# Performance work log

Measured on AMD Instinct MI355X. Metric: run time of the kernel, lower is better.

The kernel has to match this reference:

```python
import jax, jax.numpy as jnp
import numpy as np

N, E, F, H, EA = 50000, 500000, 2000, 128, 2
NUM_BOND_TYPES = 100
COORDS_RANGE = 10.0
NORM_FACTOR = 100.0


def setup_inputs() -> dict:
    key = jax.random.key(0)
    ks = jax.random.split(key, 20)

    def lin(k, i, o, gain=1.0):
        # xavier-uniform-ish init, stored as [in, out] so forward is x @ W + b
        lim = gain * np.sqrt(6.0 / (i + o))
        return jax.random.uniform(k, (i, o), jnp.float32, -lim, lim)

    inp = {
        "h_a": jax.random.normal(ks[0], (N, H), jnp.float32),
        "x_a": jax.random.normal(ks[1], (N, 3), jnp.float32),
        "e_a_idx": jax.random.randint(ks[2], (2, E), 0, N),
        "e_a_type": jax.random.randint(ks[3], (E,), 0, NUM_BOND_TYPES),
        "e_a_attr": jax.random.normal(ks[4], (E, EA), jnp.float32),
        "coord_diff_a": jax.random.normal(ks[5], (E, 3), jnp.float32),
        "h_f": jax.random.normal(ks[6], (F, H), jnp.float32),
        "x_f": jax.random.normal(ks[7], (F, 3), jnp.float32),
        "bm_mat": jax.random.normal(ks[8], (N, F), jnp.float32) / np.sqrt(F),
        # parameters
        "bond_emb": jax.random.normal(ks[9], (NUM_BOND_TYPES, H), jnp.float32),
        "aW1": lin(ks[10], 2 * H + EA + H, H), "ab1": jnp.zeros((H,), jnp.float32),
        "aW2": lin(ks[11], H, H), "ab2": jnp.zeros((H,), jnp.float32),
        "aW3": lin(ks[12], H, 1, gain=0.001),  # xavier gain=0.001, no bias
        "fW1": lin(ks[13], 2 * H + EA, H), "fb1": jnp.zeros((H,), jnp.float32),
        "fW2": lin(ks[14], H, H), "fb2": jnp.zeros((H,), jnp.float32),
        "fW3": lin(ks[15], H, 1, gain=0.001),
    }
    return inp


def reference(h_a, x_a, e_a_idx, e_a_type, e_a_attr, coord_diff_a, h_f, x_f, bm_mat,
              bond_emb, aW1, ab1, aW2, ab2, aW3, fW1, fb1, fW2, fb2, fW3):
    silu = jax.nn.silu
    row, col = e_a_idx[0], e_a_idx[1]

    be = bond_emb[e_a_type]                              # [E, H]
    coord_diff_f = x_a - bm_mat @ x_f                    # [N, 3]
    radial_f = jnp.sum(coord_diff_f ** 2, axis=1, keepdims=True)  # [N, 1]
    norm_f = jnp.sqrt(radial_f + 1e-8)
    coord_diff_f = coord_diff_f / (norm_f + 1.0)

    inp_atom = jnp.concatenate([h_a[row], h_a[col], e_a_attr, be], axis=1)        # [E, 3H+2]
    inp_frag = jnp.concatenate([h_a, bm_mat @ h_f, radial_f, radial_f], axis=1)   # [N, 2H+2]

    m_atom = silu(silu(inp_atom @ aW1 + ab1) @ aW2 + ab2) @ aW3  # [E, 1]
    m_frag = silu(silu(inp_frag @ fW1 + fb1) @ fW2 + fb2) @ fW3  # [N, 1]

    trans_atom = coord_diff_a * jnp.tanh(m_atom) * COORDS_RANGE  # [E, 3]
    trans_frag = coord_diff_f * jnp.tanh(m_frag) * COORDS_RANGE  # [N, 3]

    agg_atom = jax.ops.segment_sum(trans_atom, row, num_segments=x_a.shape[0]) / NORM_FACTOR
    return x_a + agg_atom + trans_frag
```

## Files before the change

### kernel.cpp

```cpp
#include <hip/hip_runtime.h>
#include <hip/hip_bf16.h>


typedef __attribute__((ext_vector_type(8))) short bfrag8;
typedef __attribute__((ext_vector_type(16))) float f32x16;
typedef __attribute__((ext_vector_type(4))) float f32x4v;

#define MFMA32(A, B, C) __builtin_amdgcn_mfma_f32_32x32x16_bf16((A), (B), (C), 0, 0, 0)

__device__ __forceinline__ f32x16 zero16() {
  f32x16 v;
#pragma unroll
  for (int i = 0; i < 16; ++i) v[i] = 0.0f;
  return v;
}

__device__ __forceinline__ unsigned short bf16bits(float x) {
  __hip_bfloat16 b = __float2bfloat16(x);
  unsigned short u;
  __builtin_memcpy(&u, &b, 2);
  return u;
}

__device__ __forceinline__ unsigned pk2(float lo, float hi) {
  return (unsigned)bf16bits(lo) | ((unsigned)bf16bits(hi) << 16);
}

__device__ __forceinline__ bfrag8 ldfrag(const unsigned short* p) {
  return *reinterpret_cast<const bfrag8*>(p);
}

__device__ __forceinline__ bfrag8 frag4(unsigned f0, unsigned f1, unsigned f2, unsigned f3) {
  union { unsigned u[4]; bfrag8 v; } q;
  q.u[0] = f0; q.u[1] = f1; q.u[2] = f2; q.u[3] = f3;
  return q.v;
}

__device__ __forceinline__ float silu_f(float x) { return x / (1.0f + __expf(-x)); }

__global__ __launch_bounds__(256) void prep_kernel(
    const float* __restrict__ h_a, const float* __restrict__ bond,
    const float* __restrict__ h_f,
    const float* __restrict__ aW1, const float* __restrict__ ab1,
    const float* __restrict__ aW2,
    const float* __restrict__ fW1, const float* __restrict__ fW2,
    unsigned short* __restrict__ h_bf, unsigned short* __restrict__ bond_bf,
    float* __restrict__ hfp,
    unsigned short* __restrict__ W1aT, unsigned short* __restrict__ W1bT,
    unsigned short* __restrict__ W1cT, unsigned short* __restrict__ W1eT,
    unsigned short* __restrict__ W2T,
    unsigned short* __restrict__ fW1aT, unsigned short* __restrict__ fW2T,
    float* __restrict__ agg,
    int N, int NB, int F) {
  const int t = threadIdx.x;
  int bid = blockIdx.x;
  const int G_A = (N * 16 + 255) >> 8;
  const int G_B = (NB * 16 + 255) >> 8;
  const int G_H = (F + 1) >> 1;

  if (bid < G_A + G_B) {
    const float* src = (bid < G_A) ? h_a : bond;
    unsigned short* dst = (bid < G_A) ? h_bf : bond_bf;
    int rows = (bid < G_A) ? N : NB;
    int idx = (bid < G_A ? bid : bid - G_A) * 256 + t;
    if (idx < rows * 16) {
      int row = idx >> 4, g = idx & 15;
      int h = g & 1, kc = g >> 1;
      const f32x4v* s = reinterpret_cast<const f32x4v*>(src + (size_t)row * 128 + g * 8);
      f32x4v v0 = s[0], v1 = s[1];
      unsigned* d = reinterpret_cast<unsigned*>(dst + (size_t)row * 128 + h * 64 + kc * 8);
      d[0] = pk2(v0[0], v0[1]);
      d[1] = pk2(v0[2], v0[3]);
      d[2] = pk2(v1[0], v1[1]);
      d[3] = pk2(v1[2], v1[3]);
    }
    return;
  }
  bid -= G_A + G_B;
  if (bid < G_H) {
    int f = bid * 2 + (t >> 7), n = t & 127;
    if (f < F) {
      float acc = 0.0f;
#pragma unroll 8
      for (int k = 0; k < 128; ++k)
        acc += h_f[(size_t)f * 128 + k] * fW1[(size_t)(128 + k) * 128 + n];
      hfp[(size_t)f * 128 + n] = acc;
    }
    return;
  }
  bid -= G_H;
  if (bid < 6 * 64) {
    int p = bid >> 6;
    int tt = (bid & 63) * 256 + t;
    int j = tt & 7, l = (tt >> 3) & 63, rem = tt >> 9;
    int nt = rem & 3, kc = rem >> 2;
    int k = kc * 16 + ((l >> 5) << 3) + j;
    int n = nt * 32 + (l & 31);
    const float* W;
    unsigned short* D;
    switch (p) {
      case 0: W = aW1;             D = W1aT;  break;
      case 1: W = aW1 + 128 * 128; D = W1bT;  break;
      case 2: W = aW1 + 258 * 128; D = W1cT;  break;
      case 3: W = aW2;             D = W2T;   break;
      case 4: W = fW1;             D = fW1aT; break;
      default: W = fW2;            D = fW2T;  break;
    }
    D[tt] = bf16bits(W[(size_t)k * 128 + n]);
    return;
  }
  bid -= 6 * 64;
  if (bid < 8) {
    int tt = bid * 256 + t;
    if (tt < 4 * 64 * 8) {
      int j = tt & 7, l = (tt >> 3) & 63, nt = (tt >> 9) & 3;
      int k = ((l >> 5) << 3) + j;
      int n = nt * 32 + (l & 31);
      float v = (k == 0) ? aW1[(size_t)256 * 128 + n]
              : (k == 1) ? aW1[(size_t)257 * 128 + n]
              : (k == 2) ? ab1[n] : 0.0f;
      W1eT[tt] = bf16bits(v);
    }
    return;
  }
  bid -= 8;
  {
    int i4 = (bid * 256 + t) * 4;
    if (i4 + 3 < N * 3) {
      *reinterpret_cast<f32x4v*>(agg + i4) = f32x4v{0.f, 0.f, 0.f, 0.f};
    } else {
      for (int c = 0; c < 4; ++c)
        if (i4 + c < N * 3) agg[i4 + c] = 0.0f;
    }
  }
}

__global__ void pack_bmat_kernel(const float* __restrict__ hfp, const float* __restrict__ x_f,
                                 unsigned short* __restrict__ dst, int total) {
  int t = blockIdx.x * blockDim.x + threadIdx.x;
  if (t >= total) return;
  int j = t & 7, l = (t >> 3) & 63, rem = t >> 9;
  int nt = rem % 5, kc = rem / 5;
  int k = kc * 16 + ((l >> 5) << 3) + j;
  int n = nt * 32 + (l & 31);
  float v;
  if (n < 128) v = hfp[(size_t)k * 128 + n];
  else if (n < 131) v = x_f[(size_t)k * 3 + (n - 128)];
  else v = 0.0f;
  dst[t] = bf16bits(v);
}

__global__ __launch_bounds__(256, 2) void fused_k1_k3(
    const float* __restrict__ bm, const unsigned short* __restrict__ bmT,
    float* __restrict__ k1T,
    const unsigned short* __restrict__ h_bf, const unsigned short* __restrict__ bond_bf,
    const int* __restrict__ eidx, const int* __restrict__ etype,
    const float* __restrict__ eattr, const float* __restrict__ cda,
    const unsigned short* __restrict__ W1aT, const unsigned short* __restrict__ W1bT,
    const unsigned short* __restrict__ W1cT, const unsigned short* __restrict__ W1eT,
    const unsigned short* __restrict__ W2T,
    const float* __restrict__ ab2, const float* __restrict__ aW3,
    float* __restrict__ agg,
    int N, int F, int E, int G1) {
  __shared__ __align__(16) char lds[2][128 * 128];
  const int lane = threadIdx.x & 63;
  const int w = threadIdx.x >> 6;
  const int h = lane >> 5;
  const int ln = lane & 31;

  if ((int)blockIdx.x < G1) {
    const int t = threadIdx.x;
    const int m0 = blockIdx.x * 128;
    const int NT = (F + 63) >> 6;

    f32x16 acc[5];
#pragma unroll
    for (int i = 0; i < 5; ++i) acc[i] = zero16();

    int srow[8], sch[8];
    const float* sptr[8];
#pragma unroll
    for (int p = 0; p < 8; ++p) {
      int c = p * 256 + t;
      srow[p] = c >> 4;
      sch[p] = c & 15;
      int gr = m0 + srow[p];
      if (gr >= N) gr = N - 1;
      sptr[p] = bm + (size_t)gr * F;
    }

    const int myrow = w * 32 + ln;
    const int rsw = (myrow & 7) << 4;

    f32x4v sregs[8];
#pragma unroll
    for (int p = 0; p < 8; ++p) {
      int gk = sch[p] * 4;
      if (gk > F - 4) gk = F - 4;
      sregs[p] = *reinterpret_cast<const f32x4v*>(sptr[p] + gk);
    }
#pragma unroll
    for (int p = 0; p < 8; ++p) {
      int byte = srow[p] * 128 + ((sch[p] * 8) ^ ((srow[p] & 7) << 4));
      union { unsigned u[2]; unsigned long long ull; } q;
      q.u[0] = pk2(sregs[p][0], sregs[p][1]);
      q.u[1] = pk2(sregs[p][2], sregs[p][3]);
      *reinterpret_cast<unsigned long long*>(&lds[0][byte]) = q.ull;
    }
    __syncthreads();

    int cur = 0;
    for (int kt = 0; kt < NT; ++kt) {
      const bool more = (kt + 1 < NT);
      if (more) {
#pragma unroll
        for (int p = 0; p < 8; ++p) {
          int gk = (kt + 1) * 64 + sch[p] * 4;
          if (gk > F - 4) gk = F - 4;
          sregs[p] = *reinterpret_cast<const f32x4v*>(sptr[p] + gk);
        }
      }
      const int rem = (F - kt * 64) >> 4;
      const int kcN = rem < 4 ? rem : 4;
      if (kcN == 4) {
#pragma unroll
        for (int kc = 0; kc < 4; ++kc) {
          bfrag8 b = *reinterpret_cast<const bfrag8*>(
              &lds[cur][myrow * 128 + ((kc * 32 + h * 16) ^ rsw)]);
          const unsigned short* wp = bmT + ((size_t)(kt * 4 + kc) * 5 * 64 + lane) * 8;
#pragma unroll
          for (int nt = 0; nt < 5; ++nt) acc[nt] = MFMA32(ldfrag(wp + nt * 512), b, acc[nt]);
        }
      } else {
        for (int kc = 0; kc < kcN; ++kc) {
          bfrag8 b = *reinterpret_cast<const bfrag8*>(
              &lds[cur][myrow * 128 + ((kc * 32 + h * 16) ^ rsw)]);
          const unsigned short* wp = bmT + ((size_t)(kt * 4 + kc) * 5 * 64 + lane) * 8;
#pragma unroll
          for (int nt = 0; nt < 5; ++nt) acc[nt] = MFMA32(ldfrag(wp + nt * 512), b, acc[nt]);
        }
      }
      if (more) {
#pragma unroll
        for (int p = 0; p < 8; ++p) {
          int byte = srow[p] * 128 + ((sch[p] * 8) ^ ((srow[p] & 7) << 4));
          union { unsigned u[2]; unsigned long long ull; } q;
          q.u[0] = pk2(sregs[p][0], sregs[p][1]);
          q.u[1] = pk2(sregs[p][2], sregs[p][3]);
          *reinterpret_cast<unsigned long long*>(&lds[cur ^ 1][byte]) = q.ull;
        }
      }
      __syncthreads();
      cur ^= 1;
    }

    const int m = m0 + myrow;
    if (m < N) {
#pragma unroll
      for (int nt = 0; nt < 5; ++nt)
#pragma unroll
        for (int r = 0; r < 16; ++r) {
          int n = nt * 32 + (r & 3) + 8 * (r >> 2) + 4 * h;
          if (n < 131) k1T[(size_t)n * N + m] = acc[nt][r];
        }
    }
    return;
  }

  const int e = (blockIdx.x - G1) * 128 + w * 32 + ln;
  const bool valid = (e < E);
  const int ec = valid ? e : (E - 1);
  const int row = eidx[ec];
  const int col = eidx[(size_t)E + ec];
  const int typ = etype[ec];
  const float e0 = eattr[2 * (size_t)ec];
  const float e1 = eattr[2 * (size_t)ec + 1];

  const unsigned short* hr = h_bf + (size_t)row * 128 + h * 64;
  const unsigned short* hc = h_bf + (size_t)col * 128 + h * 64;
  const unsigned short* bb = bond_bf + (size_t)typ * 128 + h * 64;

  f32x16 acc[4];
#pragma unroll
  for (int q = 0; q < 4; ++q) acc[q] = zero16();

#pragma unroll
  for (int kc = 0; kc < 8; ++kc) {
    bfrag8 b = ldfrag(hr + kc * 8);
    const unsigned short* wp = W1aT + ((size_t)(kc * 4) * 64 + lane) * 8;
#pragma unroll
    for (int nt = 0; nt < 4; ++nt) acc[nt] = MFMA32(ldfrag(wp + nt * 512), b, acc[nt]);
  }
#pragma unroll
  for (int kc = 0; kc < 8; ++kc) {
    bfrag8 b = ldfrag(hc + kc * 8);
    const unsigned short* wp = W1bT + ((size_t)(kc * 4) * 64 + lane) * 8;
#pragma unroll
    for (int nt = 0; nt < 4; ++nt) acc[nt] = MFMA32(ldfrag(wp + nt * 512), b, acc[nt]);
  }
#pragma unroll
  for (int kc = 0; kc < 8; ++kc) {
    bfrag8 b = ldfrag(bb + kc * 8);
    const unsigned short* wp = W1cT + ((size_t)(kc * 4) * 64 + lane) * 8;
#pragma unroll
    for (int nt = 0; nt < 4; ++nt) acc[nt] = MFMA32(ldfrag(wp + nt * 512), b, acc[nt]);
  }
  {
    unsigned u0 = h ? 0u : pk2(e0, e1);
    unsigned u1 = h ? 0u : 0x00003F80u;
    bfrag8 b = frag4(u0, u1, 0u, 0u);
    const unsigned short* wp = W1eT + (size_t)lane * 8;
#pragma unroll
    for (int nt = 0; nt < 4; ++nt) acc[nt] = MFMA32(ldfrag(wp + nt * 512), b, acc[nt]);
  }

  unsigned wv[32];
#pragma unroll
  for (int nt = 0; nt < 4; ++nt)
#pragma unroll
    for (int p = 0; p < 8; ++p)
      wv[nt * 8 + p] = pk2(silu_f(acc[nt][2 * p]), silu_f(acc[nt][2 * p + 1]));

#pragma unroll
  for (int q = 0; q < 4; ++q) acc[q] = zero16();
#pragma unroll
  for (int kc = 0; kc < 8; ++kc) {
    const int base = (kc >> 1) * 8 + (kc & 1) * 4;
    unsigned a0 = wv[base + 0], a1 = wv[base + 1], a2 = wv[base + 2], a3 = wv[base + 3];
    unsigned s0 = (unsigned)__shfl_xor((int)a0, 32);
    unsigned s1 = (unsigned)__shfl_xor((int)a1, 32);
    unsigned s2 = (unsigned)__shfl_xor((int)a2, 32);
    unsigned s3 = (unsigned)__shfl_xor((int)a3, 32);
    bfrag8 b = frag4(h ? s2 : a0, h ? s3 : a1, h ? a2 : s0, h ? a3 : s1);
    const unsigned short* wp = W2T + ((size_t)(kc * 4) * 64 + lane) * 8;
#pragma unroll
    for (int nt = 0; nt < 4; ++nt) acc[nt] = MFMA32(ldfrag(wp + nt * 512), b, acc[nt]);
  }

  float part = 0.0f;
#pragma unroll
  for (int nt = 0; nt < 4; ++nt)
#pragma unroll
    for (int r = 0; r < 16; ++r) {
      int n = nt * 32 + (r & 3) + 8 * (r >> 2) + 4 * h;
      part += silu_f(acc[nt][r] + ab2[n]) * aW3[n];
    }
  float mv = part + __shfl_xor(part, 32);

  if (valid) {
    float tt = tanhf(mv) * 0.1f;
    if (h == 0) {
      atomicAdd(agg + 3 * (size_t)row + 0, cda[3 * (size_t)ec + 0] * tt);
      atomicAdd(agg + 3 * (size_t)row + 1, cda[3 * (size_t)ec + 1] * tt);
    } else {
      atomicAdd(agg + 3 * (size_t)row + 2, cda[3 * (size_t)ec + 2] * tt);
    }
  }
}

__global__ __launch_bounds__(256) void k2_frag(
    const float* __restrict__ x_a, const unsigned short* __restrict__ h_bf,
    const float* __restrict__ k1T, const float* __restrict__ agg,
    const unsigned short* __restrict__ fW1aT, const unsigned short* __restrict__ fW2T,
    const float* __restrict__ fW1, const float* __restrict__ fb1,
    const float* __restrict__ fb2, const float* __restrict__ fW3,
    float* __restrict__ out, int N) {
  const int lane = threadIdx.x & 63;
  const int wid = threadIdx.x >> 6;
  const int h = lane >> 5;
  const int ln = lane & 31;
  const int i = blockIdx.x * 128 + wid * 32 + ln;
  const bool valid = (i < N);
  const int ic = valid ? i : (N - 1);

  float cd[3];
  float radial = 0.0f;
#pragma unroll
  for (int c = 0; c < 3; ++c) {
    float v = x_a[3 * (size_t)ic + c] - k1T[(size_t)(128 + c) * N + ic];
    cd[c] = v;
    radial += v * v;
  }

  f32x16 acc[4];
#pragma unroll
  for (int q = 0; q < 4; ++q) acc[q] = zero16();
  const unsigned short* hp = h_bf + (size_t)ic * 128 + h * 64;
#pragma unroll
  for (int kc = 0; kc < 8; ++kc) {
    bfrag8 b = ldfrag(hp + kc * 8);
    const unsigned short* wp = fW1aT + ((size_t)(kc * 4) * 64 + lane) * 8;
#pragma unroll
    for (int nt = 0; nt < 4; ++nt) acc[nt] = MFMA32(ldfrag(wp + nt * 512), b, acc[nt]);
  }

  unsigned wv[32];
#pragma unroll
  for (int nt = 0; nt < 4; ++nt)
#pragma unroll
    for (int p = 0; p < 8; ++p) {
      const int r0 = 2 * p;
      const int n0 = nt * 32 + (r0 & 3) + 8 * (r0 >> 2) + 4 * h;
      const int n1 = n0 + 1;
      float q0 = acc[nt][r0] + k1T[(size_t)n0 * N + ic]
               + radial * (fW1[(size_t)256 * 128 + n0] + fW1[(size_t)257 * 128 + n0]) + fb1[n0];
      float q1 = acc[nt][r0 + 1] + k1T[(size_t)n1 * N + ic]
               + radial * (fW1[(size_t)256 * 128 + n1] + fW1[(size_t)257 * 128 + n1]) + fb1[n1];
      wv[nt * 8 + p] = pk2(silu_f(q0), silu_f(q1));
    }

#pragma unroll
  for (int q = 0; q < 4; ++q) acc[q] = zero16();
#pragma unroll
  for (int kc = 0; kc < 8; ++kc) {
    const int base = (kc >> 1) * 8 + (kc & 1) * 4;
    unsigned a0 = wv[base + 0], a1 = wv[base + 1], a2 = wv[base + 2], a3 = wv[base + 3];
    unsigned s0 = (unsigned)__shfl_xor((int)a0, 32);
    unsigned s1 = (unsigned)__shfl_xor((int)a1, 32);
    unsigned s2 = (unsigned)__shfl_xor((int)a2, 32);
    unsigned s3 = (unsigned)__shfl_xor((int)a3, 32);
    bfrag8 b = frag4(h ? s2 : a0, h ? s3 : a1, h ? a2 : s0, h ? a3 : s1);
    const unsigned short* wp = fW2T + ((size_t)(kc * 4) * 64 + lane) * 8;
#pragma unroll
    for (int nt = 0; nt < 4; ++nt) acc[nt] = MFMA32(ldfrag(wp + nt * 512), b, acc[nt]);
  }

  float part = 0.0f;
#pragma unroll
  for (int nt = 0; nt < 4; ++nt)
#pragma unroll
    for (int r = 0; r < 16; ++r) {
      int n = nt * 32 + (r & 3) + 8 * (r >> 2) + 4 * h;
      part += silu_f(acc[nt][r] + fb2[n]) * fW3[n];
    }
  float mv = part + __shfl_xor(part, 32);

  if (valid && h == 0) {
    float nrm = sqrtf(radial + 1e-8f);
    float s = tanhf(mv) * 10.0f / (nrm + 1.0f);
#pragma unroll
    for (int c = 0; c < 3; ++c)
      out[3 * (size_t)i + c] = x_a[3 * (size_t)i + c] + cd[c] * s + agg[3 * (size_t)i + c];
  }
}


extern "C" void kernel_launch(void* const* d_in, const int* in_sizes, int n_in,
                              void* d_out, int out_size, void* d_ws, size_t ws_size,
                              hipStream_t stream) {
  const float* h_a    = (const float*)d_in[0];
  const float* x_a    = (const float*)d_in[1];
  const int*   e_idx  = (const int*)d_in[2];
  const int*   e_type = (const int*)d_in[3];
  const float* e_attr = (const float*)d_in[4];
  const float* cda    = (const float*)d_in[5];
  const float* h_f    = (const float*)d_in[6];
  const float* x_f    = (const float*)d_in[7];
  const float* bm     = (const float*)d_in[8];
  const float* bond   = (const float*)d_in[9];
  const float* aW1    = (const float*)d_in[10];
  const float* ab1    = (const float*)d_in[11];
  const float* aW2    = (const float*)d_in[12];
  const float* ab2    = (const float*)d_in[13];
  const float* aW3    = (const float*)d_in[14];
  const float* fW1    = (const float*)d_in[15];
  const float* fb1    = (const float*)d_in[16];
  const float* fW2    = (const float*)d_in[17];
  const float* fb2    = (const float*)d_in[18];
  const float* fW3    = (const float*)d_in[19];
  float* out = (float*)d_out;

  const int N  = in_sizes[0] / 128;
  const int E  = in_sizes[2] / 2;
  const int F  = in_sizes[6] / 128;
  const int NB = in_sizes[9] / 128;
  const int KC = F / 16;

  char* wsp = (char*)d_ws;
  size_t off = 0;
  auto alloc = [&](size_t bytes) -> char* {
    char* p = wsp + off;
    off += (bytes + 255) & ~(size_t)255;
    return p;
  };
  unsigned short* h_bf    = (unsigned short*)alloc((size_t)N * 128 * 2);
  unsigned short* bond_bf = (unsigned short*)alloc((size_t)NB * 128 * 2);
  float*          hfp     = (float*)alloc((size_t)F * 128 * 4);
  unsigned short* bmT     = (unsigned short*)alloc((size_t)KC * 5 * 64 * 8 * 2);
  unsigned short* W1aT    = (unsigned short*)alloc(8 * 4 * 64 * 8 * 2);
  unsigned short* W1bT    = (unsigned short*)alloc(8 * 4 * 64 * 8 * 2);
  unsigned short* W1cT    = (unsigned short*)alloc(8 * 4 * 64 * 8 * 2);
  unsigned short* W2T     = (unsigned short*)alloc(8 * 4 * 64 * 8 * 2);
  unsigned short* W1eT    = (unsigned short*)alloc(1 * 4 * 64 * 8 * 2);
  unsigned short* fW1aT   = (unsigned short*)alloc(8 * 4 * 64 * 8 * 2);
  unsigned short* fW2T    = (unsigned short*)alloc(8 * 4 * 64 * 8 * 2);
  float*          k1T     = (float*)alloc((size_t)131 * N * 4);
  float*          agg     = (float*)alloc((size_t)N * 3 * 4);

  const int G_A = (N * 16 + 255) >> 8;
  const int G_B = (NB * 16 + 255) >> 8;
  const int G_H = (F + 1) >> 1;
  const int G_P = 6 * 64;
  const int G_E2 = 8;
  const int G_Z = (N * 3 + 1023) >> 10;
  prep_kernel<<<G_A + G_B + G_H + G_P + G_E2 + G_Z, 256, 0, stream>>>(
      h_a, bond, h_f, aW1, ab1, aW2, fW1, fW2,
      h_bf, bond_bf, hfp, W1aT, W1bT, W1cT, W1eT, W2T, fW1aT, fW2T, agg,
      N, NB, F);

  {
    int total = KC * 5 * 64 * 8;
    pack_bmat_kernel<<<(total + 255) / 256, 256, 0, stream>>>(hfp, x_f, bmT, total);
  }

  const int G1 = (N + 127) / 128;
  const int G3 = (E + 127) / 128;
  fused_k1_k3<<<G1 + G3, 256, 0, stream>>>(
      bm, bmT, k1T,
      h_bf, bond_bf, e_idx, e_type, e_attr, cda,
      W1aT, W1bT, W1cT, W1eT, W2T, ab2, aW3, agg,
      N, F, E, G1);

  k2_frag<<<(N + 127) / 128, 256, 0, stream>>>(x_a, h_bf, k1T, agg, fW1aT, fW2T,
                                               fW1, fb1, fb2, fW3, out, N);
}
```

Measured before the change: 358.5 us.

## Split fused kernel; stage atom MLP weights in LDS with persistent edge loop

Splits the combined GEMM and edge-MLP kernel into two launches. The GEMM kernel moves to 64-row tiles with 128 threads. The edge kernel becomes persistent: 256 blocks of 512 threads each copy all W1a/W1b/W1c/W2 bf16 weight fragments (128 KB) into LDS once, then loop over edge groups, so weight loads come from LDS instead of global or L1. The trade-off is that the GEMM and edge work no longer run concurrently, only one block fits per CU because of the LDS footprint, and the code assumes the weight tables sit contiguously in memory starting at W1aT.

```diff
diff --git a/kernel.cpp b/kernel.cpp
--- a/kernel.cpp
+++ b/kernel.cpp
@@ -150,210 +150,223 @@
   dst[t] = bf16bits(v);
 }
 
-__global__ __launch_bounds__(256, 2) void fused_k1_k3(
+__global__ __launch_bounds__(128, 4) void k1_gemm(
     const float* __restrict__ bm, const unsigned short* __restrict__ bmT,
-    float* __restrict__ k1T,
+    float* __restrict__ k1T, int N, int F) {
+  __shared__ __align__(16) char lds[2][64 * 128];
+  const int t = threadIdx.x;
+  const int lane = t & 63;
+  const int w = t >> 6;
+  const int h = lane >> 5;
+  const int ln = lane & 31;
+  const int m0 = blockIdx.x * 64;
+  const int NT = (F + 63) >> 6;
+
+  f32x16 acc[5];
+#pragma unroll
+  for (int i = 0; i < 5; ++i) acc[i] = zero16();
+
+  int srow[8], sch[8];
+  const float* sptr[8];
+#pragma unroll
+  for (int p = 0; p < 8; ++p) {
+    int c = p * 128 + t;
+    srow[p] = c >> 4;
+    sch[p] = c & 15;
+    int gr = m0 + srow[p];
+    if (gr >= N) gr = N - 1;
+    sptr[p] = bm + (size_t)gr * F;
+  }
+
+  const int myrow = w * 32 + ln;
+  const int rsw = (myrow & 7) << 4;
+
+  f32x4v sregs[8];
+#pragma unroll
+  for (int p = 0; p < 8; ++p) {
+    int gk = sch[p] * 4;
+    if (gk > F - 4) gk = F - 4;
+    sregs[p] = *reinterpret_cast<const f32x4v*>(sptr[p] + gk);
+  }
+#pragma unroll
+  for (int p = 0; p < 8; ++p) {
+    int byte = srow[p] * 128 + ((sch[p] * 8) ^ ((srow[p] & 7) << 4));
+    union { unsigned u[2]; unsigned long long ull; } q;
+    q.u[0] = pk2(sregs[p][0], sregs[p][1]);
+    q.u[1] = pk2(sregs[p][2], sregs[p][3]);
+    *reinterpret_cast<unsigned long long*>(&lds[0][byte]) = q.ull;
+  }
+  __syncthreads();
+
+  int cur = 0;
+  for (int kt = 0; kt < NT; ++kt) {
+    const bool more = (kt + 1 < NT);
+    if (more) {
+#pragma unroll
+      for (int p = 0; p < 8; ++p) {
+        int gk = (kt + 1) * 64 + sch[p] * 4;
+        if (gk > F - 4) gk = F - 4;
+        sregs[p] = *reinterpret_cast<const f32x4v*>(sptr[p] + gk);
+      }
+    }
+    const int rem = (F - kt * 64) >> 4;
+    const int kcN = rem < 4 ? rem : 4;
+    if (kcN == 4) {
+#pragma unroll
+      for (int kc = 0; kc < 4; ++kc) {
+        bfrag8 b = *reinterpret_cast<const bfrag8*>(
+            &lds[cur][myrow * 128 + ((kc * 32 + h * 16) ^ rsw)]);
+        const unsigned short* wp = bmT + ((size_t)(kt * 4 + kc) * 5 * 64 + lane) * 8;
+#pragma unroll
+        for (int nt = 0; nt < 5; ++nt) acc[nt] = MFMA32(ldfrag(wp + nt * 512), b, acc[nt]);
+      }
+    } else {
+      for (int kc = 0; kc < kcN; ++kc) {
+        bfrag8 b = *reinterpret_cast<const bfrag8*>(
+            &lds[cur][myrow * 128 + ((kc * 32 + h * 16) ^ rsw)]);
+        const unsigned short* wp = bmT + ((size_t)(kt * 4 + kc) * 5 * 64 + lane) * 8;
+#pragma unroll
+        for (int nt = 0; nt < 5; ++nt) acc[nt] = MFMA32(ldfrag(wp + nt * 512), b, acc[nt]);
+      }
+    }
+    if (more) {
+#pragma unroll
+      for (int p = 0; p < 8; ++p) {
+        int byte = srow[p] * 128 + ((sch[p] * 8) ^ ((srow[p] & 7) << 4));
+        union { unsigned u[2]; unsigned long long ull; } q;
+        q.u[0] = pk2(sregs[p][0], sregs[p][1]);
+        q.u[1] = pk2(sregs[p][2], sregs[p][3]);
+        *reinterpret_cast<unsigned long long*>(&lds[cur ^ 1][byte]) = q.ull;
+      }
+    }
+    __syncthreads();
+    cur ^= 1;
+  }
+
+  const int m = m0 + myrow;
+  if (m < N) {
+#pragma unroll
+    for (int nt = 0; nt < 5; ++nt)
+#pragma unroll
+      for (int r = 0; r < 16; ++r) {
+        int n = nt * 32 + (r & 3) + 8 * (r >> 2) + 4 * h;
+        if (n < 131) k1T[(size_t)n * N + m] = acc[nt][r];
+      }
+  }
+}
+
+__global__ __launch_bounds__(512, 2) void k3_atom(
     const unsigned short* __restrict__ h_bf, const unsigned short* __restrict__ bond_bf,
+    const unsigned short* __restrict__ wtab, const unsigned short* __restrict__ W1eT,
     const int* __restrict__ eidx, const int* __restrict__ etype,
     const float* __restrict__ eattr, const float* __restrict__ cda,
-    const unsigned short* __restrict__ W1aT, const unsigned short* __restrict__ W1bT,
-    const unsigned short* __restrict__ W1cT, const unsigned short* __restrict__ W1eT,
-    const unsigned short* __restrict__ W2T,
     const float* __restrict__ ab2, const float* __restrict__ aW3,
-    float* __restrict__ agg,
-    int N, int F, int E, int G1) {
-  __shared__ __align__(16) char lds[2][128 * 128];
+    float* __restrict__ agg, int E) {
+  __shared__ __align__(16) unsigned short wlds[65536];
+  for (int i = threadIdx.x; i < 8192; i += 512)
+    reinterpret_cast<bfrag8*>(wlds)[i] = reinterpret_cast<const bfrag8*>(wtab)[i];
+  __syncthreads();
+  const unsigned short* w1a = wlds;
+  const unsigned short* w1b = wlds + 16384;
+  const unsigned short* w1c = wlds + 32768;
+  const unsigned short* w2  = wlds + 49152;
+
   const int lane = threadIdx.x & 63;
-  const int w = threadIdx.x >> 6;
+  const int wid = threadIdx.x >> 6;
   const int h = lane >> 5;
   const int ln = lane & 31;
-
-  if ((int)blockIdx.x < G1) {
-    const int t = threadIdx.x;
-    const int m0 = blockIdx.x * 128;
-    const int NT = (F + 63) >> 6;
-
-    f32x16 acc[5];
-#pragma unroll
-    for (int i = 0; i < 5; ++i) acc[i] = zero16();
-
-    int srow[8], sch[8];
-    const float* sptr[8];
-#pragma unroll
-    for (int p = 0; p < 8; ++p) {
-      int c = p * 256 + t;
-      srow[p] = c >> 4;
-      sch[p] = c & 15;
-      int gr = m0 + srow[p];
-      if (gr >= N) gr = N - 1;
-      sptr[p] = bm + (size_t)gr * F;
-    }
-
-    const int myrow = w * 32 + ln;
-    const int rsw = (myrow & 7) << 4;
-
-    f32x4v sregs[8];
-#pragma unroll
-    for (int p = 0; p < 8; ++p) {
-      int gk = sch[p] * 4;
-      if (gk > F - 4) gk = F - 4;
-      sregs[p] = *reinterpret_cast<const f32x4v*>(sptr[p] + gk);
-    }
-#pragma unroll
-    for (int p = 0; p < 8; ++p) {
-      int byte = srow[p] * 128 + ((sch[p] * 8) ^ ((srow[p] & 7) << 4));
-      union { unsigned u[2]; unsigned long long ull; } q;
-      q.u[0] = pk2(sregs[p][0], sregs[p][1]);
-      q.u[1] = pk2(sregs[p][2], sregs[p][3]);
-      *reinterpret_cast<unsigned long long*>(&lds[0][byte]) = q.ull;
-    }
-    __syncthreads();
-
-    int cur = 0;
-    for (int kt = 0; kt < NT; ++kt) {
-      const bool more = (kt + 1 < NT);
-      if (more) {
-#pragma unroll
-        for (int p = 0; p < 8; ++p) {
-          int gk = (kt + 1) * 64 + sch[p] * 4;
-          if (gk > F - 4) gk = F - 4;
-          sregs[p] = *reinterpret_cast<const f32x4v*>(sptr[p] + gk);
-        }
-      }
-      const int rem = (F - kt * 64) >> 4;
-      const int kcN = rem < 4 ? rem : 4;
-      if (kcN == 4) {
-#pragma unroll
-        for (int kc = 0; kc < 4; ++kc) {
-          bfrag8 b = *reinterpret_cast<const bfrag8*>(
-              &lds[cur][myrow * 128 + ((kc * 32 + h * 16) ^ rsw)]);
-          const unsigned short* wp = bmT + ((size_t)(kt * 4 + kc) * 5 * 64 + lane) * 8;
-#pragma unroll
-          for (int nt = 0; nt < 5; ++nt) acc[nt] = MFMA32(ldfrag(wp + nt * 512), b, acc[nt]);
-        }
+  const int nGroups = (E + 31) >> 5;
+  const int totWaves = gridDim.x * 8;
+
+  for (int g = blockIdx.x * 8 + wid; g < nGroups; g += totWaves) {
+    const int e = g * 32 + ln;
+    const bool valid = (e < E);
+    const int ec = valid ? e : (E - 1);
+    const int row = eidx[ec];
+    const int col = eidx[(size_t)E + ec];
+    const int typ = etype[ec];
+    const float e0 = eattr[2 * (size_t)ec];
+    const float e1 = eattr[2 * (size_t)ec + 1];
+
+    const unsigned short* hr = h_bf + (size_t)row * 128 + h * 64;
+    const unsigned short* hc = h_bf + (size_t)col * 128 + h * 64;
+    const unsigned short* bb = bond_bf + (size_t)typ * 128 + h * 64;
+
+    f32x16 acc[4];
+#pragma unroll
+    for (int q = 0; q < 4; ++q) acc[q] = zero16();
+
+#pragma unroll
+    for (int kc = 0; kc < 8; ++kc) {
+      bfrag8 b = ldfrag(hr + kc * 8);
+      const unsigned short* wp = w1a + ((size_t)(kc * 4) * 64 + lane) * 8;
+#pragma unroll
+      for (int nt = 0; nt < 4; ++nt) acc[nt] = MFMA32(ldfrag(wp + nt * 512), b, acc[nt]);
+    }
+#pragma unroll
+    for (int kc = 0; kc < 8; ++kc) {
+      bfrag8 b = ldfrag(hc + kc * 8);
+      const unsigned short* wp = w1b + ((size_t)(kc * 4) * 64 + lane) * 8;
+#pragma unroll
+      for (int nt = 0; nt < 4; ++nt) acc[nt] = MFMA32(ldfrag(wp + nt * 512), b, acc[nt]);
+    }
+#pragma unroll
+    for (int kc = 0; kc < 8; ++kc) {
+      bfrag8 b = ldfrag(bb + kc * 8);
+      const unsigned short* wp = w1c + ((size_t)(kc * 4) * 64 + lane) * 8;
+#pragma unroll
+      for (int nt = 0; nt < 4; ++nt) acc[nt] = MFMA32(ldfrag(wp + nt * 512), b, acc[nt]);
+    }
+    {
+      unsigned u0 = h ? 0u : pk2(e0, e1);
+      unsigned u1 = h ? 0u : 0x00003F80u;
+      bfrag8 b = frag4(u0, u1, 0u, 0u);
+      const unsigned short* wp = W1eT + (size_t)lane * 8;
+#pragma unroll
+      for (int nt = 0; nt < 4; ++nt) acc[nt] = MFMA32(ldfrag(wp + nt * 512), b, acc[nt]);
+    }
+
+    unsigned wv[32];
+#pragma unroll
+    for (int nt = 0; nt < 4; ++nt)
+#pragma unroll
+      for (int p = 0; p < 8; ++p)
+        wv[nt * 8 + p] = pk2(silu_f(acc[nt][2 * p]), silu_f(acc[nt][2 * p + 1]));
+
+#pragma unroll
+    for (int q = 0; q < 4; ++q) acc[q] = zero16();
+#pragma unroll
+    for (int kc = 0; kc < 8; ++kc) {
+      const int base = (kc >> 1) * 8 + (kc & 1) * 4;
+      unsigned a0 = wv[base + 0], a1 = wv[base + 1], a2 = wv[base + 2], a3 = wv[base + 3];
+      unsigned s0 = (unsigned)__shfl_xor((int)a0, 32);
+      unsigned s1 = (unsigned)__shfl_xor((int)a1, 32);
+      unsigned s2 = (unsigned)__shfl_xor((int)a2, 32);
+      unsigned s3 = (unsigned)__shfl_xor((int)a3, 32);
+      bfrag8 b = frag4(h ? s2 : a0, h ? s3 : a1, h ? a2 : s0, h ? a3 : s1);
+      const unsigned short* wp = w2 + ((size_t)(kc * 4) * 64 + lane) * 8;
+#pragma unroll
+      for (int nt = 0; nt < 4; ++nt) acc[nt] = MFMA32(ldfrag(wp + nt * 512), b, acc[nt]);
+    }
+
+    float part = 0.0f;
+#pragma unroll
+    for (int nt = 0; nt < 4; ++nt)
+#pragma unroll
+      for (int r = 0; r < 16; ++r) {
+        int n = nt * 32 + (r & 3) + 8 * (r >> 2) + 4 * h;
+        part += silu_f(acc[nt][r] + ab2[n]) * aW3[n];
+      }
+    float mv = part + __shfl_xor(part, 32);
+
+    if (valid) {
+      float tt = tanhf(mv) * 0.1f;
+      if (h == 0) {
+        atomicAdd(agg + 3 * (size_t)row + 0, cda[3 * (size_t)ec + 0] * tt);
+        atomicAdd(agg + 3 * (size_t)row + 1, cda[3 * (size_t)ec + 1] * tt);
       } else {
-        for (int kc = 0; kc < kcN; ++kc) {
-          bfrag8 b = *reinterpret_cast<const bfrag8*>(
-              &lds[cur][myrow * 128 + ((kc * 32 + h * 16) ^ rsw)]);
-          const unsigned short* wp = bmT + ((size_t)(kt * 4 + kc) * 5 * 64 + lane) * 8;
-#pragma unroll
-          for (int nt = 0; nt < 5; ++nt) acc[nt] = MFMA32(ldfrag(wp + nt * 512), b, acc[nt]);
-        }
-      }
-      if (more) {
-#pragma unroll
-        for (int p = 0; p < 8; ++p) {
-          int byte = srow[p] * 128 + ((sch[p] * 8) ^ ((srow[p] & 7) << 4));
-          union { unsigned u[2]; unsigned long long ull; } q;
-          q.u[0] = pk2(sregs[p][0], sregs[p][1]);
-          q.u[1] = pk2(sregs[p][2], sregs[p][3]);
-          *reinterpret_cast<unsigned long long*>(&lds[cur ^ 1][byte]) = q.ull;
-        }
-      }
-      __syncthreads();
-      cur ^= 1;
-    }
-
-    const int m = m0 + myrow;
-    if (m < N) {
-#pragma unroll
-      for (int nt = 0; nt < 5; ++nt)
-#pragma unroll
-        for (int r = 0; r < 16; ++r) {
-          int n = nt * 32 + (r & 3) + 8 * (r >> 2) + 4 * h;
-          if (n < 131) k1T[(size_t)n * N + m] = acc[nt][r];
-        }
-    }
-    return;
-  }
-
-  const int e = (blockIdx.x - G1) * 128 + w * 32 + ln;
-  const bool valid = (e < E);
-  const int ec = valid ? e : (E - 1);
-  const int row = eidx[ec];
-  const int col = eidx[(size_t)E + ec];
-  const int typ = etype[ec];
-  const float e0 = eattr[2 * (size_t)ec];
-  const float e1 = eattr[2 * (size_t)ec + 1];
-
-  const unsigned short* hr = h_bf + (size_t)row * 128 + h * 64;
-  const unsigned short* hc = h_bf + (size_t)col * 128 + h * 64;
-  const unsigned short* bb = bond_bf + (size_t)typ * 128 + h * 64;
-
-  f32x16 acc[4];
-#pragma unroll
-  for (int q = 0; q < 4; ++q) acc[q] = zero16();
-
-#pragma unroll
-  for (int kc = 0; kc < 8; ++kc) {
-    bfrag8 b = ldfrag(hr + kc * 8);
-    const unsigned short* wp = W1aT + ((size_t)(kc * 4) * 64 + lane) * 8;
-#pragma unroll
-    for (int nt = 0; nt < 4; ++nt) acc[nt] = MFMA32(ldfrag(wp + nt * 512), b, acc[nt]);
-  }
-#pragma unroll
-  for (int kc = 0; kc < 8; ++kc) {
-    bfrag8 b = ldfrag(hc + kc * 8);
-    const unsigned short* wp = W1bT + ((size_t)(kc * 4) * 64 + lane) * 8;
-#pragma unroll
-    for (int nt = 0; nt < 4; ++nt) acc[nt] = MFMA32(ldfrag(wp + nt * 512), b, acc[nt]);
-  }
-#pragma unroll
-  for (int kc = 0; kc < 8; ++kc) {
-    bfrag8 b = ldfrag(bb + kc * 8);
-    const unsigned short* wp = W1cT + ((size_t)(kc * 4) * 64 + lane) * 8;
-#pragma unroll
-    for (int nt = 0; nt < 4; ++nt) acc[nt] = MFMA32(ldfrag(wp + nt * 512), b, acc[nt]);
-  }
-  {
-    unsigned u0 = h ? 0u : pk2(e0, e1);
-    unsigned u1 = h ? 0u : 0x00003F80u;
-    bfrag8 b = frag4(u0, u1, 0u, 0u);
-    const unsigned short* wp = W1eT + (size_t)lane * 8;
-#pragma unroll
-    for (int nt = 0; nt < 4; ++nt) acc[nt] = MFMA32(ldfrag(wp + nt * 512), b, acc[nt]);
-  }
-
-  unsigned wv[32];
-#pragma unroll
-  for (int nt = 0; nt < 4; ++nt)
-#pragma unroll
-    for (int p = 0; p < 8; ++p)
-      wv[nt * 8 + p] = pk2(silu_f(acc[nt][2 * p]), silu_f(acc[nt][2 * p + 1]));
-
-#pragma unroll
-  for (int q = 0; q < 4; ++q) acc[q] = zero16();
-#pragma unroll
-  for (int kc = 0; kc < 8; ++kc) {
-    const int base = (kc >> 1) * 8 + (kc & 1) * 4;
-    unsigned a0 = wv[base + 0], a1 = wv[base + 1], a2 = wv[base + 2], a3 = wv[base + 3];
-    unsigned s0 = (unsigned)__shfl_xor((int)a0, 32);
-    unsigned s1 = (unsigned)__shfl_xor((int)a1, 32);
-    unsigned s2 = (unsigned)__shfl_xor((int)a2, 32);
-    unsigned s3 = (unsigned)__shfl_xor((int)a3, 32);
-    bfrag8 b = frag4(h ? s2 : a0, h ? s3 : a1, h ? a2 : s0, h ? a3 : s1);
-    const unsigned short* wp = W2T + ((size_t)(kc * 4) * 64 + lane) * 8;
-#pragma unroll
-    for (int nt = 0; nt < 4; ++nt) acc[nt] = MFMA32(ldfrag(wp + nt * 512), b, acc[nt]);
-  }
-
-  float part = 0.0f;
-#pragma unroll
-  for (int nt = 0; nt < 4; ++nt)
-#pragma unroll
-    for (int r = 0; r < 16; ++r) {
-      int n = nt * 32 + (r & 3) + 8 * (r >> 2) + 4 * h;
-      part += silu_f(acc[nt][r] + ab2[n]) * aW3[n];
-    }
-  float mv = part + __shfl_xor(part, 32);
-
-  if (valid) {
-    float tt = tanhf(mv) * 0.1f;
-    if (h == 0) {
-      atomicAdd(agg + 3 * (size_t)row + 0, cda[3 * (size_t)ec + 0] * tt);
-      atomicAdd(agg + 3 * (size_t)row + 1, cda[3 * (size_t)ec + 1] * tt);
-    } else {
-      atomicAdd(agg + 3 * (size_t)row + 2, cda[3 * (size_t)ec + 2] * tt);
+        atomicAdd(agg + 3 * (size_t)row + 2, cda[3 * (size_t)ec + 2] * tt);
+      }
     }
   }
 }
@@ -513,13 +526,10 @@
     pack_bmat_kernel<<<(total + 255) / 256, 256, 0, stream>>>(hfp, x_f, bmT, total);
   }
 
-  const int G1 = (N + 127) / 128;
-  const int G3 = (E + 127) / 128;
-  fused_k1_k3<<<G1 + G3, 256, 0, stream>>>(
-      bm, bmT, k1T,
-      h_bf, bond_bf, e_idx, e_type, e_attr, cda,
-      W1aT, W1bT, W1cT, W1eT, W2T, ab2, aW3, agg,
-      N, F, E, G1);
+  k1_gemm<<<(N + 63) / 64, 128, 0, stream>>>(bm, bmT, k1T, N, F);
+
+  k3_atom<<<256, 512, 0, stream>>>(h_bf, bond_bf, W1aT, W1eT,
+                                   e_idx, e_type, e_attr, cda, ab2, aW3, agg, E);
 
   k2_frag<<<(N + 127) / 128, 256, 0, stream>>>(x_a, h_bf, k1T, agg, fW1aT, fW2T,
                                                fW1, fb1, fb2, fW3, out, N);
```

New measurement: 1.429 ms. +298.5%, slower.
